# Optimization experiments

Measured on AMD Instinct MI355X. Metric: run time of the kernel, lower is better.

## Reference

```python
import jax, jax.numpy as jnp
import numpy as np

B, L, C = 1, 4096, 1024
H = 16
D = C // H  # head_dim = 64


def setup_inputs() -> dict:
    key = jax.random.key(0)
    k1, k2, k3 = jax.random.split(key, 3)
    scale_in = 1.0 / np.sqrt(C)
    return {
        "x": jax.random.normal(k1, (B, L, C), dtype=jnp.float32),
        "Wqkv": jax.random.normal(k2, (C, 3 * C), dtype=jnp.float32) * scale_in,
        "bqkv": jnp.zeros((3 * C,), dtype=jnp.float32),
        "Wout": jax.random.normal(k3, (C, C), dtype=jnp.float32) * scale_in,
        "bout": jnp.zeros((C,), dtype=jnp.float32),
    }


def reference(x, Wqkv, bqkv, Wout, bout):
    Bx, Lx, Cx = x.shape
    qkv = x @ Wqkv + bqkv                             # [B, L, 3C]
    qkv = qkv.reshape(Bx, Lx, 3, H, D)
    qkv = jnp.transpose(qkv, (2, 0, 3, 1, 4))         # [3, B, H, L, D]
    q, k, v = qkv[0], qkv[1], qkv[2]
    scores = jnp.einsum("bhqd,bhkd->bhqk", q, k) / jnp.sqrt(jnp.float32(D))
    # causal mask: strictly upper triangle -> -inf
    causal = jnp.triu(jnp.ones((Lx, Lx), dtype=bool), k=1)
    scores = jnp.where(causal, -jnp.inf, scores)
    attn = jax.nn.softmax(scores, axis=-1)            # [B, H, L, L]
    out = jnp.einsum("bhqk,bhkd->bhqd", attn, v)      # [B, H, L, D]
    out = jnp.transpose(out, (0, 2, 1, 3)).reshape(Bx, Lx, Cx)
    return out @ Wout + bout
```

## Files before the change

kernel.cpp:

```cpp
#include <hip/hip_runtime.h>
#include <hip/hip_bf16.h>

typedef unsigned short u16;
typedef __bf16 bf16x8 __attribute__((ext_vector_type(8)));
typedef float f32x4 __attribute__((ext_vector_type(4)));

#define L_SEQ 4096
#define CDIM  1024
#define NH    16
#define HD    64
#define N_QKV 3072
#define ATT_STRIDE 88

static __device__ __forceinline__ float bf2f(u16 u) {
    union { float f; unsigned int i; } v; v.i = ((unsigned int)u) << 16; return v.f;
}
static __device__ __forceinline__ u16 f2bf(float f) {
    union { float f; unsigned int i; } v; v.f = f;
    unsigned int u = v.i;
    return (u16)((u + 0x7fffu + ((u >> 16) & 1u)) >> 16);
}

static __device__ __forceinline__ f32x4 mfma16x16x32(bf16x8 a, bf16x8 b, f32x4 c) {
    return __builtin_amdgcn_mfma_f32_16x16x32_bf16(a, b, c, 0, 0, 0);
}

typedef const __attribute__((address_space(1))) unsigned int* gas_u32;
typedef __attribute__((address_space(3))) unsigned int* las_u32;
static __device__ __forceinline__ void gload_lds16(const u16* g, u16* l) {
    __builtin_amdgcn_global_load_lds((gas_u32)g, (las_u32)l, 16, 0, 0);
}

__global__ __launch_bounds__(256) void k_cast_x(const float* __restrict__ src,
                                                u16* __restrict__ dst, int n8) {
    int i = blockIdx.x * 256 + threadIdx.x;
    if (i >= n8) return;
    const float4* s = (const float4*)(src + (size_t)i * 8);
    float4 a = s[0], b = s[1];
    u16 o[8] = { f2bf(a.x), f2bf(a.y), f2bf(a.z), f2bf(a.w),
                 f2bf(b.x), f2bf(b.y), f2bf(b.z), f2bf(b.w) };
    *(uint4*)(dst + (size_t)i * 8) = *(uint4*)o;
}

__global__ __launch_bounds__(256) void k_transpose_cast(const float* __restrict__ src,
                                                        u16* __restrict__ dst,
                                                        int R, int C) {
    __shared__ u16 tile[32][33];
    int c0 = blockIdx.x * 32, r0 = blockIdx.y * 32;
    int tx = threadIdx.x & 31, ty = threadIdx.x >> 5;
#pragma unroll
    for (int i = 0; i < 32; i += 8)
        tile[ty + i][tx] = f2bf(src[(size_t)(r0 + ty + i) * C + c0 + tx]);
    __syncthreads();
#pragma unroll
    for (int i = 0; i < 32; i += 8)
        dst[(size_t)(c0 + ty + i) * R + r0 + tx] = tile[tx][ty + i];
}

__global__ __launch_bounds__(256) void k_transpose_v(const u16* __restrict__ qkv,
                                                     u16* __restrict__ vt) {
    __shared__ u16 tile[32][33];
    int k0 = blockIdx.x * 32, d0 = blockIdx.y * 32, h = blockIdx.z;
    int tx = threadIdx.x & 31, ty = threadIdx.x >> 5;
#pragma unroll
    for (int i = 0; i < 32; i += 8)
        tile[ty + i][tx] = qkv[(size_t)(k0 + ty + i) * N_QKV + 2 * CDIM + h * HD + d0 + tx];
    __syncthreads();
#pragma unroll
    for (int i = 0; i < 32; i += 8)
        vt[(size_t)(h * HD + d0 + ty + i) * L_SEQ + k0 + tx] = tile[tx][ty + i];
}

template <typename OutT>
__global__ __launch_bounds__(256) void k_gemm_bt(const u16* __restrict__ A,
                                                 const u16* __restrict__ Bt,
                                                 const float* __restrict__ bias,
                                                 OutT* __restrict__ Cmat,
                                                 int M, int N, int K) {
    __shared__ alignas(16) u16 As[128 * 32];
    __shared__ alignas(16) u16 Bs[128 * 32];
    int t = threadIdx.x;
    int n0 = blockIdx.x * 128, m0 = blockIdx.y * 128;
    int l = t & 63, w = t >> 6;
    int wm = (w >> 1) * 64, wn = (w & 1) * 64;
    int lr = l & 15, lq = l >> 4;

    const f32x4 vzero = {0.f, 0.f, 0.f, 0.f};
    f32x4 acc[4][4];
#pragma unroll
    for (int mi = 0; mi < 4; mi++)
#pragma unroll
        for (int ni = 0; ni < 4; ni++) acc[mi][ni] = vzero;

    int ar = t >> 2;
    int ac = (t & 3) * 8;
    const u16* Ag = A + (size_t)(m0 + ar) * K + ac;
    const u16* Bg = Bt + (size_t)(n0 + ar) * K + ac;
    u16* AsD0 = &As[t * 8];
    u16* AsD1 = &As[t * 8 + 64 * 32];
    u16* BsD0 = &Bs[t * 8];
    u16* BsD1 = &Bs[t * 8 + 64 * 32];

    for (int k0 = 0; k0 < K; k0 += 32) {
        gload_lds16(Ag + k0,                     AsD0);
        gload_lds16(Ag + (size_t)64 * K + k0,    AsD1);
        gload_lds16(Bg + k0,                     BsD0);
        gload_lds16(Bg + (size_t)64 * K + k0,    BsD1);
        __syncthreads();

        bf16x8 af[4], bfr[4];
#pragma unroll
        for (int mi = 0; mi < 4; mi++)
            af[mi] = *(const bf16x8*)&As[(wm + mi * 16 + lr) * 32 + lq * 8];
#pragma unroll
        for (int ni = 0; ni < 4; ni++)
            bfr[ni] = *(const bf16x8*)&Bs[(wn + ni * 16 + lr) * 32 + lq * 8];
#pragma unroll
        for (int mi = 0; mi < 4; mi++)
#pragma unroll
            for (int ni = 0; ni < 4; ni++)
                acc[mi][ni] = mfma16x16x32(af[mi], bfr[ni], acc[mi][ni]);
        __syncthreads();
    }

#pragma unroll
    for (int ni = 0; ni < 4; ni++) {
        int col = n0 + wn + ni * 16 + lr;
        float bv = bias[col];
#pragma unroll
        for (int mi = 0; mi < 4; mi++) {
            int row = m0 + wm + mi * 16 + lq * 4;
#pragma unroll
            for (int r = 0; r < 4; r++) {
                float v = acc[mi][ni][r] + bv;
                if constexpr (sizeof(OutT) == 2)
                    Cmat[(size_t)(row + r) * N + col] = f2bf(v);
                else
                    Cmat[(size_t)(row + r) * N + col] = v;
            }
        }
    }
}

__global__ __launch_bounds__(512, 4) void k_attn(const u16* __restrict__ qkv,
                                                 const u16* __restrict__ vt,
                                                 u16* __restrict__ attn) {
    __shared__ alignas(16) u16 Ks[2][64 * ATT_STRIDE];
    __shared__ alignas(16) u16 Vs[2][64 * ATT_STRIDE];

    int t = threadIdx.x;
    int l = t & 63, w = t >> 6;
    int g = w >> 2;
    int ww = w & 3;
    int h = blockIdx.y;
    int lr = l & 15, lq = l >> 4;
    int tg = t & 255;
    int row8 = tg >> 3;
    int ch = (tg & 7) * 8;
    int qloc = ww * 16 + lr;

    const f32x4 vzero = {0.f, 0.f, 0.f, 0.f};
    const u16* Kbase = qkv + (size_t)row8 * N_QKV + CDIM + h * HD + ch;
    const u16* Vbase = vt + (size_t)(h * HD + row8) * L_SEQ + ch;
    u16* KsG = Ks[g];
    u16* VsG = Vs[g];

#pragma unroll
    for (int phase = 0; phase < 2; phase++) {
        int tile = phase ? (63 - blockIdx.x) : blockIdx.x;
        int q0 = tile * 64;
        int nkv = tile + 1;
        int h0 = (nkv + 1) >> 1;
        int myBeg = g ? h0 : 0;
        int myCnt = g ? (nkv - h0) : h0;

        bf16x8 bq[2];
        {
            const u16* Qg = qkv + (size_t)(q0 + qloc) * N_QKV + h * HD + lq * 8;
            union { uint4 u; u16 hh[8]; } q0u, q1u;
            q0u.u = *(const uint4*)(Qg);
            q1u.u = *(const uint4*)(Qg + 32);
            union { bf16x8 v; u16 hh[8]; } f0, f1;
#pragma unroll
            for (int j = 0; j < 8; j++) {
                f0.hh[j] = f2bf(bf2f(q0u.hh[j]) * 0.125f);
                f1.hh[j] = f2bf(bf2f(q1u.hh[j]) * 0.125f);
            }
            bq[0] = f0.v; bq[1] = f1.v;
        }

        f32x4 o[4];
#pragma unroll
        for (int dt = 0; dt < 4; dt++) o[dt] = vzero;
        float m_i = -1e30f, l_i = 0.f;

        uint4 rk0 = {0,0,0,0}, rk1 = {0,0,0,0}, rv0 = {0,0,0,0}, rv1 = {0,0,0,0};
        if (myCnt > 0) {
            const u16* Kg = Kbase + (size_t)(myBeg * 64) * N_QKV;
            rk0 = *(const uint4*)Kg;
            rk1 = *(const uint4*)(Kg + (size_t)32 * N_QKV);
            const u16* Vg = Vbase + myBeg * 64;
            rv0 = *(const uint4*)Vg;
            rv1 = *(const uint4*)(Vg + (size_t)32 * L_SEQ);
        }

        for (int it = 0; it < h0; ++it) {
            bool act = it < myCnt;
            if (act) {
                *(uint4*)&KsG[row8 * ATT_STRIDE + ch]        = rk0;
                *(uint4*)&KsG[(row8 + 32) * ATT_STRIDE + ch] = rk1;
                *(uint4*)&VsG[row8 * ATT_STRIDE + ch]        = rv0;
                *(uint4*)&VsG[(row8 + 32) * ATT_STRIDE + ch] = rv1;
            }
            __syncthreads();

            if (it + 1 < myCnt) {
                int k1 = (myBeg + it + 1) * 64;
                const u16* Kg = Kbase + (size_t)k1 * N_QKV;
                rk0 = *(const uint4*)Kg;
                rk1 = *(const uint4*)(Kg + (size_t)32 * N_QKV);
                const u16* Vg = Vbase + k1;
                rv0 = *(const uint4*)Vg;
                rv1 = *(const uint4*)(Vg + (size_t)32 * L_SEQ);
            }

            if (act) {
                f32x4 s[4];
#pragma unroll
                for (int nt = 0; nt < 4; nt++) s[nt] = vzero;
#pragma unroll
                for (int ks = 0; ks < 2; ks++)
#pragma unroll
                    for (int nt = 0; nt < 4; nt++) {
                        bf16x8 ak = *(const bf16x8*)&KsG[(nt * 16 + lr) * ATT_STRIDE + ks * 32 + lq * 8];
                        s[nt] = mfma16x16x32(ak, bq[ks], s[nt]);
                    }

                bool diag = (((myBeg + it) * 64) == q0);
                float tmax = -1e30f;
#pragma unroll
                for (int nt = 0; nt < 4; nt++)
#pragma unroll
                    for (int r = 0; r < 4; r++) {
                        float v = s[nt][r];
                        if (diag && (nt * 16 + lq * 4 + r > qloc)) v = -1e30f;
                        s[nt][r] = v;
                        tmax = fmaxf(tmax, v);
                    }
                tmax = fmaxf(tmax, __shfl_xor(tmax, 16));
                tmax = fmaxf(tmax, __shfl_xor(tmax, 32));

                float mnew = fmaxf(m_i, tmax);
                float alpha = __expf(m_i - mnew);
                float rsum = 0.f;
#pragma unroll
                for (int nt = 0; nt < 4; nt++)
#pragma unroll
                    for (int r = 0; r < 4; r++) {
                        float e = __expf(s[nt][r] - mnew);
                        s[nt][r] = e;
                        rsum += e;
                    }
                rsum += __shfl_xor(rsum, 16);
                rsum += __shfl_xor(rsum, 32);
                l_i = l_i * alpha + rsum;
                m_i = mnew;
#pragma unroll
                for (int dt = 0; dt < 4; dt++)
#pragma unroll
                    for (int r = 0; r < 4; r++) o[dt][r] *= alpha;

#pragma unroll
                for (int a = 0; a < 2; a++) {
                    union { bf16x8 v; u16 hh[8]; } bp;
#pragma unroll
                    for (int r = 0; r < 4; r++) {
                        bp.hh[r]     = f2bf(s[2 * a][r]);
                        bp.hh[r + 4] = f2bf(s[2 * a + 1][r]);
                    }
#pragma unroll
                    for (int dt = 0; dt < 4; dt++) {
                        union { bf16x8 v; uint2 u2[2]; } av;
                        const u16* vrow = &VsG[(dt * 16 + lr) * ATT_STRIDE + a * 32 + lq * 4];
                        av.u2[0] = *(const uint2*)(vrow);
                        av.u2[1] = *(const uint2*)(vrow + 16);
                        o[dt] = mfma16x16x32(av.v, bp.v, o[dt]);
                    }
                }
            }
            __syncthreads();
        }

        float* mb1 = (float*)Ks[1];
        float* mb2 = (float*)Vs[1];
        if (g == 1) {
            float* p = mb1 + tg * 10;
            p[0] = m_i; p[1] = l_i;
#pragma unroll
            for (int r = 0; r < 4; r++) { p[2 + r] = o[0][r]; p[6 + r] = o[1][r]; }
            float* p2 = mb2 + tg * 8;
#pragma unroll
            for (int r = 0; r < 4; r++) { p2[r] = o[2][r]; p2[4 + r] = o[3][r]; }
        }
        __syncthreads();
        if (g == 0) {
            float* p = mb1 + tg * 10;
            float m1v = p[0], l1v = p[1];
            float mnew = fmaxf(m_i, m1v);
            float a0 = __expf(m_i - mnew);
            float a1 = __expf(m1v - mnew);
            float lm = l_i * a0 + l1v * a1;
            float* p2 = mb2 + tg * 8;
            f32x4 o1[4];
#pragma unroll
            for (int r = 0; r < 4; r++) {
                o1[0][r] = p[2 + r]; o1[1][r] = p[6 + r];
                o1[2][r] = p2[r];    o1[3][r] = p2[4 + r];
            }
            float inv = 1.0f / lm;
            int qg = q0 + qloc;
#pragma unroll
            for (int dt = 0; dt < 4; dt++) {
                union { u16 hh[4]; uint2 u2; } eo;
#pragma unroll
                for (int r = 0; r < 4; r++)
                    eo.hh[r] = f2bf((o[dt][r] * a0 + o1[dt][r] * a1) * inv);
                *(uint2*)&attn[(size_t)qg * CDIM + h * HD + dt * 16 + lq * 4] = eo.u2;
            }
        }
        __syncthreads();
    }
}

extern "C" void kernel_launch(void* const* d_in, const int* in_sizes, int n_in,
                              void* d_out, int out_size, void* d_ws, size_t ws_size,
                              hipStream_t stream) {
    const float* x    = (const float*)d_in[0];
    const float* Wqkv = (const float*)d_in[1];
    const float* bqkv = (const float*)d_in[2];
    const float* Wout = (const float*)d_in[3];
    const float* bout = (const float*)d_in[4];
    float* out = (float*)d_out;

    char* ws = (char*)d_ws;
    u16* qkv   = (u16*)(ws);
    u16* xb    = (u16*)(ws + 25165824);
    u16* attn  = xb;
    u16* vt    = (u16*)(ws + 33554432);
    u16* wqkvt = (u16*)(ws + 41943040);
    u16* woutt = (u16*)(ws + 48234496);

    k_cast_x<<<dim3(2048), 256, 0, stream>>>(x, xb, 524288);
    k_transpose_cast<<<dim3(96, 32), 256, 0, stream>>>(Wqkv, wqkvt, 1024, 3072);
    k_transpose_cast<<<dim3(32, 32), 256, 0, stream>>>(Wout, woutt, 1024, 1024);
    k_gemm_bt<u16><<<dim3(24, 32), 256, 0, stream>>>(xb, wqkvt, bqkv, qkv, 4096, 3072, 1024);
    k_transpose_v<<<dim3(128, 2, 16), 256, 0, stream>>>(qkv, vt);
    k_attn<<<dim3(32, 16), 512, 0, stream>>>(qkv, vt, attn);
    k_gemm_bt<float><<<dim3(8, 32), 256, 0, stream>>>(attn, woutt, bout, out, 4096, 1024, 1024);
}
```

Baseline: 236.6 us.

## Double-buffer attention K/V tiles with lazy rescaling and priority hints

Gives the attention kernel two LDS buffers for K/V, so the next tile is written while the current one is consumed. This removes one barrier-bound store/sync stall per iteration, and the row stride shrinks to keep total LDS in check. It also adds conditional online-softmax rescaling (skipped unless the max grows by more than 8), a separate path for non-diagonal masking, s_setprio around the MFMA blocks, native __bf16 conversions, and a swapped grid order so heads vary along blockIdx.x. Lazy rescaling can let exponentials grow up to e^8 before normalization, and stride 72 may change LDS bank-conflict behaviour.

```diff
diff --git a/kernel.cpp b/kernel.cpp
--- a/kernel.cpp
+++ b/kernel.cpp
@@ -10,7 +10,8 @@
 #define NH    16
 #define HD    64
 #define N_QKV 3072
-#define ATT_STRIDE 88
+#define ATT_STRIDE 72
+#define TILE_HW (64 * ATT_STRIDE)
 
 static __device__ __forceinline__ float bf2f(u16 u) {
     union { float f; unsigned int i; } v; v.i = ((unsigned int)u) << 16; return v.f;
@@ -145,14 +146,15 @@
 __global__ __launch_bounds__(512, 4) void k_attn(const u16* __restrict__ qkv,
                                                  const u16* __restrict__ vt,
                                                  u16* __restrict__ attn) {
-    __shared__ alignas(16) u16 Ks[2][64 * ATT_STRIDE];
-    __shared__ alignas(16) u16 Vs[2][64 * ATT_STRIDE];
+    __shared__ alignas(16) u16 Ks[2][2 * TILE_HW];
+    __shared__ alignas(16) u16 Vs[2][2 * TILE_HW];
 
     int t = threadIdx.x;
     int l = t & 63, w = t >> 6;
     int g = w >> 2;
     int ww = w & 3;
-    int h = blockIdx.y;
+    int h = blockIdx.x;
+    int pair = blockIdx.y;
     int lr = l & 15, lq = l >> 4;
     int tg = t & 255;
     int row8 = tg >> 3;
@@ -167,7 +169,7 @@
 
 #pragma unroll
     for (int phase = 0; phase < 2; phase++) {
-        int tile = phase ? (63 - blockIdx.x) : blockIdx.x;
+        int tile = phase ? (63 - pair) : pair;
         int q0 = tile * 64;
         int nkv = tile + 1;
         int h0 = (nkv + 1) >> 1;
@@ -180,11 +182,11 @@
             union { uint4 u; u16 hh[8]; } q0u, q1u;
             q0u.u = *(const uint4*)(Qg);
             q1u.u = *(const uint4*)(Qg + 32);
-            union { bf16x8 v; u16 hh[8]; } f0, f1;
+            union { bf16x8 v; __bf16 e[8]; } f0, f1;
 #pragma unroll
             for (int j = 0; j < 8; j++) {
-                f0.hh[j] = f2bf(bf2f(q0u.hh[j]) * 0.125f);
-                f1.hh[j] = f2bf(bf2f(q1u.hh[j]) * 0.125f);
+                f0.e[j] = (__bf16)(bf2f(q0u.hh[j]) * 0.125f);
+                f1.e[j] = (__bf16)(bf2f(q1u.hh[j]) * 0.125f);
             }
             bq[0] = f0.v; bq[1] = f1.v;
         }
@@ -202,20 +204,33 @@
             const u16* Vg = Vbase + myBeg * 64;
             rv0 = *(const uint4*)Vg;
             rv1 = *(const uint4*)(Vg + (size_t)32 * L_SEQ);
-        }
-
-        for (int it = 0; it < h0; ++it) {
-            bool act = it < myCnt;
-            if (act) {
-                *(uint4*)&KsG[row8 * ATT_STRIDE + ch]        = rk0;
-                *(uint4*)&KsG[(row8 + 32) * ATT_STRIDE + ch] = rk1;
-                *(uint4*)&VsG[row8 * ATT_STRIDE + ch]        = rv0;
-                *(uint4*)&VsG[(row8 + 32) * ATT_STRIDE + ch] = rv1;
-            }
-            __syncthreads();
-
-            if (it + 1 < myCnt) {
-                int k1 = (myBeg + it + 1) * 64;
+            *(uint4*)&KsG[row8 * ATT_STRIDE + ch]        = rk0;
+            *(uint4*)&KsG[(row8 + 32) * ATT_STRIDE + ch] = rk1;
+            *(uint4*)&VsG[row8 * ATT_STRIDE + ch]        = rv0;
+            *(uint4*)&VsG[(row8 + 32) * ATT_STRIDE + ch] = rv1;
+            if (myCnt > 1) {
+                int k1 = (myBeg + 1) * 64;
+                Kg = Kbase + (size_t)k1 * N_QKV;
+                rk0 = *(const uint4*)Kg;
+                rk1 = *(const uint4*)(Kg + (size_t)32 * N_QKV);
+                Vg = Vbase + k1;
+                rv0 = *(const uint4*)Vg;
+                rv1 = *(const uint4*)(Vg + (size_t)32 * L_SEQ);
+            }
+        }
+        __syncthreads();
+
+        for (int j = 0; j < h0; ++j) {
+            int cur = (j & 1) ? TILE_HW : 0;
+            if (j + 1 < myCnt) {
+                int nxt = TILE_HW - cur;
+                *(uint4*)&KsG[nxt + row8 * ATT_STRIDE + ch]        = rk0;
+                *(uint4*)&KsG[nxt + (row8 + 32) * ATT_STRIDE + ch] = rk1;
+                *(uint4*)&VsG[nxt + row8 * ATT_STRIDE + ch]        = rv0;
+                *(uint4*)&VsG[nxt + (row8 + 32) * ATT_STRIDE + ch] = rv1;
+            }
+            if (j + 2 < myCnt) {
+                int k1 = (myBeg + j + 2) * 64;
                 const u16* Kg = Kbase + (size_t)k1 * N_QKV;
                 rk0 = *(const uint4*)Kg;
                 rk1 = *(const uint4*)(Kg + (size_t)32 * N_QKV);
@@ -224,69 +239,87 @@
                 rv1 = *(const uint4*)(Vg + (size_t)32 * L_SEQ);
             }
 
-            if (act) {
+            if (j < myCnt) {
+                const u16* Kc = KsG + cur;
+                const u16* Vc = VsG + cur;
+
                 f32x4 s[4];
 #pragma unroll
                 for (int nt = 0; nt < 4; nt++) s[nt] = vzero;
+                __builtin_amdgcn_s_setprio(1);
 #pragma unroll
                 for (int ks = 0; ks < 2; ks++)
 #pragma unroll
                     for (int nt = 0; nt < 4; nt++) {
-                        bf16x8 ak = *(const bf16x8*)&KsG[(nt * 16 + lr) * ATT_STRIDE + ks * 32 + lq * 8];
+                        bf16x8 ak = *(const bf16x8*)&Kc[(nt * 16 + lr) * ATT_STRIDE + ks * 32 + lq * 8];
                         s[nt] = mfma16x16x32(ak, bq[ks], s[nt]);
                     }
-
-                bool diag = (((myBeg + it) * 64) == q0);
+                __builtin_amdgcn_s_setprio(0);
+
+                bool diag = (((myBeg + j) * 64) == q0);
                 float tmax = -1e30f;
-#pragma unroll
-                for (int nt = 0; nt < 4; nt++)
-#pragma unroll
-                    for (int r = 0; r < 4; r++) {
-                        float v = s[nt][r];
-                        if (diag && (nt * 16 + lq * 4 + r > qloc)) v = -1e30f;
-                        s[nt][r] = v;
-                        tmax = fmaxf(tmax, v);
-                    }
+                if (diag) {
+#pragma unroll
+                    for (int nt = 0; nt < 4; nt++)
+#pragma unroll
+                        for (int r = 0; r < 4; r++) {
+                            float v = s[nt][r];
+                            if (nt * 16 + lq * 4 + r > qloc) v = -1e30f;
+                            s[nt][r] = v;
+                            tmax = fmaxf(tmax, v);
+                        }
+                } else {
+#pragma unroll
+                    for (int nt = 0; nt < 4; nt++)
+#pragma unroll
+                        for (int r = 0; r < 4; r++) tmax = fmaxf(tmax, s[nt][r]);
+                }
                 tmax = fmaxf(tmax, __shfl_xor(tmax, 16));
                 tmax = fmaxf(tmax, __shfl_xor(tmax, 32));
 
-                float mnew = fmaxf(m_i, tmax);
-                float alpha = __expf(m_i - mnew);
+                if (!__all(tmax <= m_i + 8.0f)) {
+                    float mnew = fmaxf(m_i, tmax);
+                    float alpha = __expf(m_i - mnew);
+                    l_i *= alpha;
+#pragma unroll
+                    for (int dt = 0; dt < 4; dt++)
+#pragma unroll
+                        for (int r = 0; r < 4; r++) o[dt][r] *= alpha;
+                    m_i = mnew;
+                }
+
                 float rsum = 0.f;
 #pragma unroll
                 for (int nt = 0; nt < 4; nt++)
 #pragma unroll
                     for (int r = 0; r < 4; r++) {
-                        float e = __expf(s[nt][r] - mnew);
+                        float e = __expf(s[nt][r] - m_i);
                         s[nt][r] = e;
                         rsum += e;
                     }
                 rsum += __shfl_xor(rsum, 16);
                 rsum += __shfl_xor(rsum, 32);
-                l_i = l_i * alpha + rsum;
-                m_i = mnew;
-#pragma unroll
-                for (int dt = 0; dt < 4; dt++)
-#pragma unroll
-                    for (int r = 0; r < 4; r++) o[dt][r] *= alpha;
-
+                l_i += rsum;
+
+                __builtin_amdgcn_s_setprio(1);
 #pragma unroll
                 for (int a = 0; a < 2; a++) {
-                    union { bf16x8 v; u16 hh[8]; } bp;
+                    union { bf16x8 v; __bf16 e[8]; } bp;
 #pragma unroll
                     for (int r = 0; r < 4; r++) {
-                        bp.hh[r]     = f2bf(s[2 * a][r]);
-                        bp.hh[r + 4] = f2bf(s[2 * a + 1][r]);
+                        bp.e[r]     = (__bf16)s[2 * a][r];
+                        bp.e[r + 4] = (__bf16)s[2 * a + 1][r];
                     }
 #pragma unroll
                     for (int dt = 0; dt < 4; dt++) {
                         union { bf16x8 v; uint2 u2[2]; } av;
-                        const u16* vrow = &VsG[(dt * 16 + lr) * ATT_STRIDE + a * 32 + lq * 4];
+                        const u16* vrow = &Vc[(dt * 16 + lr) * ATT_STRIDE + a * 32 + lq * 4];
                         av.u2[0] = *(const uint2*)(vrow);
                         av.u2[1] = *(const uint2*)(vrow + 16);
                         o[dt] = mfma16x16x32(av.v, bp.v, o[dt]);
                     }
                 }
+                __builtin_amdgcn_s_setprio(0);
             }
             __syncthreads();
         }
@@ -321,10 +354,10 @@
             int qg = q0 + qloc;
 #pragma unroll
             for (int dt = 0; dt < 4; dt++) {
-                union { u16 hh[4]; uint2 u2; } eo;
+                union { u16 hh[4]; uint2 u2; __bf16 e[4]; } eo;
 #pragma unroll
                 for (int r = 0; r < 4; r++)
-                    eo.hh[r] = f2bf((o[dt][r] * a0 + o1[dt][r] * a1) * inv);
+                    eo.e[r] = (__bf16)((o[dt][r] * a0 + o1[dt][r] * a1) * inv);
                 *(uint2*)&attn[(size_t)qg * CDIM + h * HD + dt * 16 + lq * 4] = eo.u2;
             }
         }
@@ -355,6 +388,6 @@
     k_transpose_cast<<<dim3(32, 32), 256, 0, stream>>>(Wout, woutt, 1024, 1024);
     k_gemm_bt<u16><<<dim3(24, 32), 256, 0, stream>>>(xb, wqkvt, bqkv, qkv, 4096, 3072, 1024);
     k_transpose_v<<<dim3(128, 2, 16), 256, 0, stream>>>(qkv, vt);
-    k_attn<<<dim3(32, 16), 512, 0, stream>>>(qkv, vt, attn);
+    k_attn<<<dim3(16, 32), 512, 0, stream>>>(qkv, vt, attn);
     k_gemm_bt<float><<<dim3(8, 32), 256, 0, stream>>>(attn, woutt, bout, out, 4096, 1024, 1024);
 }
```

After: 228.6 us. -3.4%, faster.
